# Kernel optimization log

Measured on AMD Instinct MI355X. Metric: run time of the kernel, lower is better.

The kernel has to match this reference:

```python
import jax, jax.numpy as jnp
import numpy as np

NUM_HEAD = 16
EMB_DIM = 1024
HEAD_DIM = EMB_DIM // NUM_HEAD

def setup_inputs() -> dict:
    key = jax.random.key(0)
    ks = jax.random.split(key, 9)
    B, S, D = 2, 2048, EMB_DIM
    s = 1.0 / np.sqrt(D)
    return {
        "x": jax.random.normal(ks[0], (B, S, D), dtype=jnp.float32),
        "Wq": jax.random.normal(ks[1], (D, D), dtype=jnp.float32) * s,
        "bq": jnp.zeros((D,), dtype=jnp.float32),
        "Wk": jax.random.normal(ks[2], (D, D), dtype=jnp.float32) * s,
        "bk": jnp.zeros((D,), dtype=jnp.float32),
        "Wv": jax.random.normal(ks[3], (D, D), dtype=jnp.float32) * s,
        "bv": jnp.zeros((D,), dtype=jnp.float32),
        "Wo": jax.random.normal(ks[4], (D, D), dtype=jnp.float32) * s,
        "bo": jnp.zeros((D,), dtype=jnp.float32),
    }

def reference(x, Wq, bq, Wk, bk, Wv, bv, Wo, bo):
    B, S, D = x.shape
    H, Hd = NUM_HEAD, HEAD_DIM
    # projections (torch Linear: x @ W.T + b; here W stored as [in, out])
    Q = (x @ Wq + bq).reshape(B, S, H, Hd)
    K = (x @ Wk + bk).reshape(B, S, H, Hd)
    V = (x @ Wv + bv).reshape(B, S, H, Hd)
    scale = jnp.sqrt(jnp.asarray(Hd, dtype=x.dtype))
    scores = jnp.einsum('bqhd,bkhd->bhqk', Q, K) / scale  # [B,H,S,S]
    attn = jax.nn.softmax(scores, axis=-1)
    out = jnp.einsum('bhql,blhd->bqhd', attn, V).reshape(B, S, D)
    return out @ Wo + bo
```

## Files before the change

kernel.cpp:

```cpp
#include <hip/hip_runtime.h>
#include <math.h>


using bf16   = __bf16;
using bf16x8 = __attribute__((ext_vector_type(8))) __bf16;
using bf16x4 = __attribute__((ext_vector_type(4))) __bf16;
using f32x4  = __attribute__((ext_vector_type(4))) float;

#define MFMA16(a, b, c) __builtin_amdgcn_mfma_f32_16x16x32_bf16((a), (b), (c), 0, 0, 0)
#define WAIT_VM0() asm volatile("s_waitcnt vmcnt(0)" ::: "memory")

__device__ __forceinline__ bf16x8 ld8(const bf16* p) { return *(const bf16x8*)p; }

__device__ __forceinline__ void ldg_lds16(bf16* lds_base, const bf16* g) {
    __builtin_amdgcn_global_load_lds(
        (const __attribute__((address_space(1))) void*)g,
        (__attribute__((address_space(3))) void*)lds_base, 16, 0, 0);
}

__device__ __forceinline__ float fast_exp2(float x) {
#if __has_builtin(__builtin_amdgcn_exp2f)
    return __builtin_amdgcn_exp2f(x);
#else
    return exp2f(x);
#endif
}

__device__ __forceinline__ float rowsum16(float v) {
    v += __shfl_xor(v, 1, 64);
    v += __shfl_xor(v, 2, 64);
    v += __shfl_xor(v, 4, 64);
    v += __shfl_xor(v, 8, 64);
    return v;
}

__global__ __launch_bounds__(256) void convert_x_kernel(const float* __restrict__ x,
                                                        bf16* __restrict__ xb) {
    int i = (blockIdx.x * 256 + threadIdx.x) * 4;
    float4 v = *(const float4*)&x[i];
    bf16x4 o = { (bf16)v.x, (bf16)v.y, (bf16)v.z, (bf16)v.w };
    *(bf16x4*)&xb[i] = o;
}

__global__ __launch_bounds__(256) void transpose_w_kernel(
    const float* __restrict__ Wq, const float* __restrict__ Wk,
    const float* __restrict__ Wv, const float* __restrict__ Wo,
    bf16* __restrict__ WtBase) {
    __shared__ float tile[32][33];
    const int z = blockIdx.z;
    const float* W = (z == 0) ? Wq : (z == 1) ? Wk : (z == 2) ? Wv : Wo;
    bf16* Wt = WtBase + (size_t)z * 1024 * 1024;
    const int tx = threadIdx.x, ty = threadIdx.y;
    const int x0 = blockIdx.x * 32, y0 = blockIdx.y * 32;
#pragma unroll
    for (int i = 0; i < 4; ++i)
        tile[ty + i * 8][tx] = W[(size_t)(y0 + ty + i * 8) * 1024 + x0 + tx];
    __syncthreads();
#pragma unroll
    for (int i = 0; i < 4; ++i)
        Wt[(size_t)(x0 + ty + i * 8) * 1024 + y0 + tx] = (bf16)tile[tx][ty + i * 8];
}

__device__ __forceinline__ void gemm_stage(const bf16* __restrict__ src, int r0,
                                           int k0, bf16* dst, int w, int lane) {
#pragma unroll
    for (int c = 0; c < 2; ++c) {
        int flat = (w * 2 + c) * 64 + lane;
        int row = flat >> 2, cc = flat & 3;
        int gk = (cc ^ ((row >> 1) & 3)) * 8;
        ldg_lds16(dst + (size_t)(w * 2 + c) * 512,
                  src + (size_t)(r0 + row) * 1024 + k0 + gk);
    }
}

__device__ __forceinline__ void gemm_core_128(const bf16* __restrict__ A,
                                              const bf16* __restrict__ Bt,
                                              int m0, int n0,
                                              bf16* As, bf16* Bs,
                                              f32x4 (&acc)[4][4]) {
    const int tid = threadIdx.x, lane = tid & 63, w = tid >> 6;
    const int lo = lane & 15, quad = lane >> 4;
    const int wm = w >> 1, wn = w & 1;

    gemm_stage(A,  m0, 0, As, w, lane);
    gemm_stage(Bt, n0, 0, Bs, w, lane);
    WAIT_VM0();
    __syncthreads();

    for (int it = 0; it < 32; ++it) {
        const int buf = it & 1;
        if (it + 1 < 32) {
            gemm_stage(A,  m0, (it + 1) * 32, As + (buf ^ 1) * 4096, w, lane);
            gemm_stage(Bt, n0, (it + 1) * 32, Bs + (buf ^ 1) * 4096, w, lane);
        }
        const bf16* Ab = As + buf * 4096;
        const bf16* Bb = Bs + buf * 4096;
        bf16x8 af[4], bq[4];
#pragma unroll
        for (int t = 0; t < 4; ++t) {
            int r = wm * 64 + t * 16 + lo;
            af[t] = ld8(&Ab[r * 32 + ((quad ^ ((r >> 1) & 3)) * 8)]);
        }
#pragma unroll
        for (int t = 0; t < 4; ++t) {
            int r = wn * 64 + t * 16 + lo;
            bq[t] = ld8(&Bb[r * 32 + ((quad ^ ((r >> 1) & 3)) * 8)]);
        }
#pragma unroll
        for (int mt = 0; mt < 4; ++mt)
#pragma unroll
            for (int nt = 0; nt < 4; ++nt)
                acc[mt][nt] = MFMA16(af[mt], bq[nt], acc[mt][nt]);
        WAIT_VM0();
        __syncthreads();
    }
}

__global__ __launch_bounds__(256, 3) void qkv_gemm_kernel(
    const bf16* __restrict__ Xb, const bf16* __restrict__ Wts,
    const float* __restrict__ bq, const float* __restrict__ bk,
    const float* __restrict__ bv,
    bf16* __restrict__ Qo, bf16* __restrict__ Ko, bf16* __restrict__ Vto) {
    __shared__ bf16 As[2 * 4096];
    __shared__ bf16 Bs[2 * 4096];
    const int z = blockIdx.z;
    const bf16*  Bt   = Wts + (size_t)z * 1024 * 1024;
    const float* bias = (z == 0) ? bq : (z == 1) ? bk : bv;
    const int m0 = blockIdx.y * 128, n0 = blockIdx.x * 128;

    f32x4 acc[4][4] = {};
    gemm_core_128(Xb, Bt, m0, n0, As, Bs, acc);

    const int lane = threadIdx.x & 63, w = threadIdx.x >> 6;
    const int lo = lane & 15, quad = lane >> 4;
    const int wm = w >> 1, wn = w & 1;
    const float QSCALE = 0.125f * 1.44269504088896f;
#pragma unroll
    for (int mt = 0; mt < 4; ++mt)
#pragma unroll
        for (int nt = 0; nt < 4; ++nt)
#pragma unroll
            for (int r = 0; r < 4; ++r) {
                int m = m0 + wm * 64 + mt * 16 + quad * 4 + r;
                int n = n0 + wn * 64 + nt * 16 + lo;
                float v = acc[mt][nt][r] + bias[n];
                int b = m >> 11, s = m & 2047, h = n >> 6, hd = n & 63;
                if (z == 0)
                    Qo[((size_t)((b * 16 + h) * 2048 + s) << 6) + hd] = (bf16)(v * QSCALE);
                else if (z == 1)
                    Ko[((size_t)((b * 16 + h) * 2048 + s) << 6) + hd] = (bf16)v;
                else
                    Vto[((size_t)((b * 16 + h) * 64 + hd) << 11) + s] = (bf16)v;
            }
}

__global__ __launch_bounds__(256, 3) void out_gemm_kernel(
    const bf16* __restrict__ Ab, const bf16* __restrict__ Bt,
    const float* __restrict__ bo, float* __restrict__ Co) {
    __shared__ bf16 As[2 * 4096];
    __shared__ bf16 Bs[2 * 4096];
    const int m0 = blockIdx.y * 128, n0 = blockIdx.x * 128;
    f32x4 acc[4][4] = {};
    gemm_core_128(Ab, Bt, m0, n0, As, Bs, acc);

    const int lane = threadIdx.x & 63, w = threadIdx.x >> 6;
    const int lo = lane & 15, quad = lane >> 4;
    const int wm = w >> 1, wn = w & 1;
#pragma unroll
    for (int mt = 0; mt < 4; ++mt)
#pragma unroll
        for (int nt = 0; nt < 4; ++nt)
#pragma unroll
            for (int r = 0; r < 4; ++r) {
                int m = m0 + wm * 64 + mt * 16 + quad * 4 + r;
                int n = n0 + wn * 64 + nt * 16 + lo;
                Co[(size_t)m * 1024 + n] = acc[mt][nt][r] + bo[n];
            }
}

#define PSTRIDE 72

__global__ __launch_bounds__(256, 2) void attn_kernel(
    const bf16* __restrict__ Q, const bf16* __restrict__ K,
    const bf16* __restrict__ Vt, bf16* __restrict__ AO) {
    __shared__ bf16 Ks[2][64 * 64];
    __shared__ bf16 Vs[2][64 * 64];
    __shared__ bf16 Pl[4][32 * PSTRIDE];
    const int tid = threadIdx.x, w = tid >> 6, lane = tid & 63;
    const int lo = lane & 15, quad = lane >> 4;
    const int blk = blockIdx.x;
    const int bh = (blk & 7) | ((blk >> 7) << 3);
    const int qb = (blk >> 3) & 15;
    const int q0 = qb * 128 + w * 32;

    const bf16* Qb = Q + ((size_t)bh * 2048 + q0) * 64;
    const bf16* Kb = K + (size_t)bh * 2048 * 64;
    const bf16* Vb = Vt + (size_t)bh * 64 * 2048;
    bf16* Pw = &Pl[w][0];

    bf16x8 qa[2][2];
#pragma unroll
    for (int mt = 0; mt < 2; ++mt)
#pragma unroll
        for (int ks = 0; ks < 2; ++ks)
            qa[mt][ks] = ld8(&Qb[(mt * 16 + lo) * 64 + ks * 32 + quad * 8]);

    f32x4 O[2][4] = {};
    f32x4 l_acc[2] = {};

    auto stage = [&](int s0, int buf) {
#pragma unroll
        for (int c = 0; c < 2; ++c) {
            int flat = (w * 2 + c) * 64 + lane;
            int row = flat >> 3, cc = flat & 7;
            int gK = (cc ^ ((row >> 2) & 7)) * 8;
            int gV = (cc ^ (row & 7)) * 8;
            ldg_lds16(&Ks[buf][(w * 2 + c) * 512], &Kb[(size_t)(s0 + row) * 64 + gK]);
            ldg_lds16(&Vs[buf][(w * 2 + c) * 512], &Vb[(size_t)row * 2048 + s0 + gV]);
        }
    };

    stage(0, 0);
    WAIT_VM0();
    __syncthreads();

    for (int it = 0; it < 32; ++it) {
        const int buf = it & 1;
        if (it + 1 < 32) stage((it + 1) * 64, buf ^ 1);
        const bf16* Kt = &Ks[buf][0];
        const bf16* Vl = &Vs[buf][0];

        f32x4 S[2][4] = {};
#pragma unroll
        for (int t = 0; t < 4; ++t) {
            int r = lo * 4 + t;
#pragma unroll
            for (int ks = 0; ks < 2; ++ks) {
                bf16x8 kf = ld8(&Kt[r * 64 + (((quad + 4 * ks) ^ ((r >> 2) & 7)) * 8)]);
                S[0][t] = MFMA16(qa[0][ks], kf, S[0][t]);
                S[1][t] = MFMA16(qa[1][ks], kf, S[1][t]);
            }
        }
#pragma unroll
        for (int mt = 0; mt < 2; ++mt)
#pragma unroll
            for (int r = 0; r < 4; ++r) {
                float p0 = fast_exp2(S[mt][0][r]);
                float p1 = fast_exp2(S[mt][1][r]);
                float p2 = fast_exp2(S[mt][2][r]);
                float p3 = fast_exp2(S[mt][3][r]);
                l_acc[mt][r] += (p0 + p1) + (p2 + p3);
                bf16x4 pk = { (bf16)p0, (bf16)p1, (bf16)p2, (bf16)p3 };
                *(bf16x4*)&Pw[(mt * 16 + quad * 4 + r) * PSTRIDE + lo * 4] = pk;
            }
#pragma unroll
        for (int mt = 0; mt < 2; ++mt) {
            bf16x8 pa0 = ld8(&Pw[(mt * 16 + lo) * PSTRIDE + quad * 8]);
            bf16x8 pa1 = ld8(&Pw[(mt * 16 + lo) * PSTRIDE + 32 + quad * 8]);
#pragma unroll
            for (int nt = 0; nt < 4; ++nt) {
                int r = nt * 16 + lo;
                bf16x8 v0 = ld8(&Vl[r * 64 + ((quad ^ (r & 7)) * 8)]);
                bf16x8 v1 = ld8(&Vl[r * 64 + (((quad + 4) ^ (r & 7)) * 8)]);
                O[mt][nt] = MFMA16(pa0, v0, O[mt][nt]);
                O[mt][nt] = MFMA16(pa1, v1, O[mt][nt]);
            }
        }
        WAIT_VM0();
        __syncthreads();
    }

    const int bb = bh >> 4, h = bh & 15;
#pragma unroll
    for (int mt = 0; mt < 2; ++mt) {
        const size_t outbase = ((size_t)(bb * 2048 + q0 + mt * 16)) * 1024 + h * 64;
#pragma unroll
        for (int r = 0; r < 4; ++r) {
            float rl = 1.0f / rowsum16(l_acc[mt][r]);
            size_t rowoff = outbase + (size_t)(quad * 4 + r) * 1024;
#pragma unroll
            for (int nt = 0; nt < 4; ++nt)
                AO[rowoff + nt * 16 + lo] = (bf16)(O[mt][nt][r] * rl);
        }
    }
}

extern "C" void kernel_launch(void* const* d_in, const int* in_sizes, int n_in,
                              void* d_out, int out_size, void* d_ws, size_t ws_size,
                              hipStream_t stream) {
    const float* x  = (const float*)d_in[0];
    const float* Wq = (const float*)d_in[1];
    const float* bq = (const float*)d_in[2];
    const float* Wk = (const float*)d_in[3];
    const float* bk = (const float*)d_in[4];
    const float* Wv = (const float*)d_in[5];
    const float* bv = (const float*)d_in[6];
    const float* Wo = (const float*)d_in[7];
    const float* bo = (const float*)d_in[8];
    float* out = (float*)d_out;

    bf16* wsb = (bf16*)d_ws;
    const size_t M1 = 1024u * 1024u;
    bf16* Xb  = wsb;
    bf16* AO  = wsb;
    bf16* Wt  = wsb + 4 * M1;
    bf16* Qw  = wsb + 8 * M1;
    bf16* Kw  = wsb + 12 * M1;
    bf16* Vtw = wsb + 16 * M1;

    convert_x_kernel<<<4096, 256, 0, stream>>>(x, Xb);
    transpose_w_kernel<<<dim3(32, 32, 4), dim3(32, 8), 0, stream>>>(Wq, Wk, Wv, Wo, Wt);
    qkv_gemm_kernel<<<dim3(8, 32, 3), 256, 0, stream>>>(Xb, Wt, bq, bk, bv, Qw, Kw, Vtw);
    attn_kernel<<<512, 256, 0, stream>>>(Qw, Kw, Vtw, AO);
    out_gemm_kernel<<<dim3(8, 32), 256, 0, stream>>>(AO, Wt + 3 * M1, bo, out);
}
```

Before: 203.7 us.

## Split attention into 128-thread blocks with shared V fragments and smaller P buffer

The attention kernel now runs 1024 blocks of two waves (64 query rows each) instead of 512 blocks of four waves. Each wave stages more of the K/V tile itself, and its probability scratch shrinks to one 16-row slab with a 68-element stride. That slab is reused for both 16-row halves. The V fragments are loaded from LDS once and reused for both halves, which cuts LDS reads. The cost is that every K/V tile is loaded from global memory by twice as many blocks, with fewer waves per block to hide latency.

```diff
diff --git a/kernel.cpp b/kernel.cpp
--- a/kernel.cpp
+++ b/kernel.cpp
@@ -178,20 +178,20 @@
             }
 }
 
-#define PSTRIDE 72
-
-__global__ __launch_bounds__(256, 2) void attn_kernel(
+#define PSTR 68
+
+__global__ __launch_bounds__(128, 2) void attn_kernel(
     const bf16* __restrict__ Q, const bf16* __restrict__ K,
     const bf16* __restrict__ Vt, bf16* __restrict__ AO) {
     __shared__ bf16 Ks[2][64 * 64];
     __shared__ bf16 Vs[2][64 * 64];
-    __shared__ bf16 Pl[4][32 * PSTRIDE];
+    __shared__ bf16 Pl[2][16 * PSTR];
     const int tid = threadIdx.x, w = tid >> 6, lane = tid & 63;
     const int lo = lane & 15, quad = lane >> 4;
     const int blk = blockIdx.x;
-    const int bh = (blk & 7) | ((blk >> 7) << 3);
-    const int qb = (blk >> 3) & 15;
-    const int q0 = qb * 128 + w * 32;
+    const int bh = (blk & 7) | ((blk >> 8) << 3);
+    const int qt = (blk >> 3) & 31;
+    const int q0 = qt * 64 + w * 32;
 
     const bf16* Qb = Q + ((size_t)bh * 2048 + q0) * 64;
     const bf16* Kb = K + (size_t)bh * 2048 * 64;
@@ -210,13 +210,14 @@
 
     auto stage = [&](int s0, int buf) {
 #pragma unroll
-        for (int c = 0; c < 2; ++c) {
-            int flat = (w * 2 + c) * 64 + lane;
+        for (int c = 0; c < 4; ++c) {
+            int slot = w * 4 + c;
+            int flat = slot * 64 + lane;
             int row = flat >> 3, cc = flat & 7;
             int gK = (cc ^ ((row >> 2) & 7)) * 8;
             int gV = (cc ^ (row & 7)) * 8;
-            ldg_lds16(&Ks[buf][(w * 2 + c) * 512], &Kb[(size_t)(s0 + row) * 64 + gK]);
-            ldg_lds16(&Vs[buf][(w * 2 + c) * 512], &Vb[(size_t)row * 2048 + s0 + gV]);
+            ldg_lds16(&Ks[buf][slot * 512], &Kb[(size_t)(s0 + row) * 64 + gK]);
+            ldg_lds16(&Vs[buf][slot * 512], &Vb[(size_t)row * 2048 + s0 + gV]);
         }
     };
 
@@ -242,28 +243,51 @@
             }
         }
 #pragma unroll
-        for (int mt = 0; mt < 2; ++mt)
-#pragma unroll
-            for (int r = 0; r < 4; ++r) {
-                float p0 = fast_exp2(S[mt][0][r]);
-                float p1 = fast_exp2(S[mt][1][r]);
-                float p2 = fast_exp2(S[mt][2][r]);
-                float p3 = fast_exp2(S[mt][3][r]);
-                l_acc[mt][r] += (p0 + p1) + (p2 + p3);
-                bf16x4 pk = { (bf16)p0, (bf16)p1, (bf16)p2, (bf16)p3 };
-                *(bf16x4*)&Pw[(mt * 16 + quad * 4 + r) * PSTRIDE + lo * 4] = pk;
-            }
-#pragma unroll
-        for (int mt = 0; mt < 2; ++mt) {
-            bf16x8 pa0 = ld8(&Pw[(mt * 16 + lo) * PSTRIDE + quad * 8]);
-            bf16x8 pa1 = ld8(&Pw[(mt * 16 + lo) * PSTRIDE + 32 + quad * 8]);
+        for (int r = 0; r < 4; ++r) {
+            float p0 = fast_exp2(S[0][0][r]);
+            float p1 = fast_exp2(S[0][1][r]);
+            float p2 = fast_exp2(S[0][2][r]);
+            float p3 = fast_exp2(S[0][3][r]);
+            l_acc[0][r] += (p0 + p1) + (p2 + p3);
+            bf16x4 pk = { (bf16)p0, (bf16)p1, (bf16)p2, (bf16)p3 };
+            *(bf16x4*)&Pw[(quad * 4 + r) * PSTR + lo * 4] = pk;
+        }
+        bf16x4 pk1[4];
+#pragma unroll
+        for (int r = 0; r < 4; ++r) {
+            float p0 = fast_exp2(S[1][0][r]);
+            float p1 = fast_exp2(S[1][1][r]);
+            float p2 = fast_exp2(S[1][2][r]);
+            float p3 = fast_exp2(S[1][3][r]);
+            l_acc[1][r] += (p0 + p1) + (p2 + p3);
+            pk1[r] = bf16x4{ (bf16)p0, (bf16)p1, (bf16)p2, (bf16)p3 };
+        }
+        bf16x8 vf0[4], vf1[4];
+#pragma unroll
+        for (int nt = 0; nt < 4; ++nt) {
+            int r = nt * 16 + lo;
+            vf0[nt] = ld8(&Vl[r * 64 + ((quad ^ (r & 7)) * 8)]);
+            vf1[nt] = ld8(&Vl[r * 64 + (((quad + 4) ^ (r & 7)) * 8)]);
+        }
+        {
+            bf16x8 pa0 = ld8(&Pw[lo * PSTR + quad * 8]);
+            bf16x8 pa1 = ld8(&Pw[lo * PSTR + 32 + quad * 8]);
 #pragma unroll
             for (int nt = 0; nt < 4; ++nt) {
-                int r = nt * 16 + lo;
-                bf16x8 v0 = ld8(&Vl[r * 64 + ((quad ^ (r & 7)) * 8)]);
-                bf16x8 v1 = ld8(&Vl[r * 64 + (((quad + 4) ^ (r & 7)) * 8)]);
-                O[mt][nt] = MFMA16(pa0, v0, O[mt][nt]);
-                O[mt][nt] = MFMA16(pa1, v1, O[mt][nt]);
+                O[0][nt] = MFMA16(pa0, vf0[nt], O[0][nt]);
+                O[0][nt] = MFMA16(pa1, vf1[nt], O[0][nt]);
+            }
+        }
+#pragma unroll
+        for (int r = 0; r < 4; ++r)
+            *(bf16x4*)&Pw[(quad * 4 + r) * PSTR + lo * 4] = pk1[r];
+        {
+            bf16x8 pa0 = ld8(&Pw[lo * PSTR + quad * 8]);
+            bf16x8 pa1 = ld8(&Pw[lo * PSTR + 32 + quad * 8]);
+#pragma unroll
+            for (int nt = 0; nt < 4; ++nt) {
+                O[1][nt] = MFMA16(pa0, vf0[nt], O[1][nt]);
+                O[1][nt] = MFMA16(pa1, vf1[nt], O[1][nt]);
             }
         }
         WAIT_VM0();
@@ -311,6 +335,6 @@
     convert_x_kernel<<<4096, 256, 0, stream>>>(x, Xb);
     transpose_w_kernel<<<dim3(32, 32, 4), dim3(32, 8), 0, stream>>>(Wq, Wk, Wv, Wo, Wt);
     qkv_gemm_kernel<<<dim3(8, 32, 3), 256, 0, stream>>>(Xb, Wt, bq, bk, bv, Qw, Kw, Vtw);
-    attn_kernel<<<512, 256, 0, stream>>>(Qw, Kw, Vtw, AO);
+    attn_kernel<<<1024, 128, 0, stream>>>(Qw, Kw, Vtw, AO);
     out_gemm_kernel<<<dim3(8, 32), 256, 0, stream>>>(AO, Wt + 3 * M1, bo, out);
 }
```

New measurement: 220.7 us. +8.3%, slower.

## Stage V-transpose epilogue through LDS and use 64-row tiles for output GEMM

Applied to the files above, without the earlier changes.

In the QKV projection, the V output (stored transposed) is now written by first staging each 64-row half of the tile transposed in shared memory, then emitting contiguous 4-element vector stores along the sequence dimension. This replaces scattered 2-byte strided stores. The output projection GEMM now uses a 64x128 tile with its own double-buffered loop, which doubles the grid to 512 blocks so the device's CUs are better covered. The trade-off is extra barriers and LDS traffic in the QKV epilogue, and less reuse per block in the output GEMM.

```diff
diff --git a/kernel.cpp b/kernel.cpp
--- a/kernel.cpp
+++ b/kernel.cpp
@@ -121,8 +121,9 @@
     const float* __restrict__ bq, const float* __restrict__ bk,
     const float* __restrict__ bv,
     bf16* __restrict__ Qo, bf16* __restrict__ Ko, bf16* __restrict__ Vto) {
-    __shared__ bf16 As[2 * 4096];
-    __shared__ bf16 Bs[2 * 4096];
+    __shared__ bf16 Smem[4 * 4096];
+    bf16* As = Smem;
+    bf16* Bs = Smem + 2 * 4096;
     const int z = blockIdx.z;
     const bf16*  Bt   = Wts + (size_t)z * 1024 * 1024;
     const float* bias = (z == 0) ? bq : (z == 1) ? bk : bv;
@@ -131,48 +132,129 @@
     f32x4 acc[4][4] = {};
     gemm_core_128(Xb, Bt, m0, n0, As, Bs, acc);
 
-    const int lane = threadIdx.x & 63, w = threadIdx.x >> 6;
+    const int tid = threadIdx.x;
+    const int lane = tid & 63, w = tid >> 6;
     const int lo = lane & 15, quad = lane >> 4;
     const int wm = w >> 1, wn = w & 1;
     const float QSCALE = 0.125f * 1.44269504088896f;
-#pragma unroll
-    for (int mt = 0; mt < 4; ++mt)
-#pragma unroll
-        for (int nt = 0; nt < 4; ++nt)
-#pragma unroll
-            for (int r = 0; r < 4; ++r) {
-                int m = m0 + wm * 64 + mt * 16 + quad * 4 + r;
-                int n = n0 + wn * 64 + nt * 16 + lo;
-                float v = acc[mt][nt][r] + bias[n];
-                int b = m >> 11, s = m & 2047, h = n >> 6, hd = n & 63;
-                if (z == 0)
-                    Qo[((size_t)((b * 16 + h) * 2048 + s) << 6) + hd] = (bf16)(v * QSCALE);
-                else if (z == 1)
-                    Ko[((size_t)((b * 16 + h) * 2048 + s) << 6) + hd] = (bf16)v;
-                else
-                    Vto[((size_t)((b * 16 + h) * 64 + hd) << 11) + s] = (bf16)v;
-            }
-}
-
-__global__ __launch_bounds__(256, 3) void out_gemm_kernel(
-    const bf16* __restrict__ Ab, const bf16* __restrict__ Bt,
+
+    if (z == 2) {
+        bf16* T = Smem;
+        const int b = m0 >> 11;
+        const int s_base = m0 & 2047;
+#pragma unroll
+        for (int half = 0; half < 2; ++half) {
+            __syncthreads();
+            if (wm == half) {
+#pragma unroll
+                for (int nt = 0; nt < 4; ++nt)
+#pragma unroll
+                    for (int mt = 0; mt < 4; ++mt)
+#pragma unroll
+                        for (int r = 0; r < 4; ++r) {
+                            int nn = wn * 64 + nt * 16 + lo;
+                            int mm = mt * 16 + quad * 4 + r;
+                            T[nn * 68 + mm] = (bf16)(acc[mt][nt][r] + bias[n0 + nn]);
+                        }
+            }
+            __syncthreads();
+#pragma unroll
+            for (int p = 0; p < 8; ++p) {
+                int pos = p * 1024 + tid * 4;
+                int row = pos >> 6, col = pos & 63;
+                int n = n0 + row, h = n >> 6, hd = n & 63;
+                bf16x4 v = *(const bf16x4*)&T[row * 68 + col];
+                *(bf16x4*)&Vto[((size_t)((b * 16 + h) * 64 + hd) << 11)
+                               + s_base + half * 64 + col] = v;
+            }
+        }
+    } else {
+#pragma unroll
+        for (int mt = 0; mt < 4; ++mt)
+#pragma unroll
+            for (int nt = 0; nt < 4; ++nt)
+#pragma unroll
+                for (int r = 0; r < 4; ++r) {
+                    int m = m0 + wm * 64 + mt * 16 + quad * 4 + r;
+                    int n = n0 + wn * 64 + nt * 16 + lo;
+                    float v = acc[mt][nt][r] + bias[n];
+                    int b = m >> 11, s = m & 2047, h = n >> 6, hd = n & 63;
+                    if (z == 0)
+                        Qo[((size_t)((b * 16 + h) * 2048 + s) << 6) + hd] = (bf16)(v * QSCALE);
+                    else
+                        Ko[((size_t)((b * 16 + h) * 2048 + s) << 6) + hd] = (bf16)v;
+                }
+    }
+}
+
+__global__ __launch_bounds__(256, 2) void out_gemm_kernel(
+    const bf16* __restrict__ A, const bf16* __restrict__ Bt,
     const float* __restrict__ bo, float* __restrict__ Co) {
-    __shared__ bf16 As[2 * 4096];
+    __shared__ bf16 As[2 * 2048];
     __shared__ bf16 Bs[2 * 4096];
-    const int m0 = blockIdx.y * 128, n0 = blockIdx.x * 128;
-    f32x4 acc[4][4] = {};
-    gemm_core_128(Ab, Bt, m0, n0, As, Bs, acc);
-
-    const int lane = threadIdx.x & 63, w = threadIdx.x >> 6;
+    const int tid = threadIdx.x, lane = tid & 63, w = tid >> 6;
     const int lo = lane & 15, quad = lane >> 4;
     const int wm = w >> 1, wn = w & 1;
-#pragma unroll
-    for (int mt = 0; mt < 4; ++mt)
+    const int m0 = blockIdx.y * 64, n0 = blockIdx.x * 128;
+
+    auto stageA = [&](int k0, bf16* dst) {
+        int flat = w * 64 + lane;
+        int row = flat >> 2, cc = flat & 3;
+        int gk = (cc ^ ((row >> 1) & 3)) * 8;
+        ldg_lds16(dst + (size_t)w * 512, A + (size_t)(m0 + row) * 1024 + k0 + gk);
+    };
+    auto stageB = [&](int k0, bf16* dst) {
+#pragma unroll
+        for (int c = 0; c < 2; ++c) {
+            int flat = (w * 2 + c) * 64 + lane;
+            int row = flat >> 2, cc = flat & 3;
+            int gk = (cc ^ ((row >> 1) & 3)) * 8;
+            ldg_lds16(dst + (size_t)(w * 2 + c) * 512,
+                      Bt + (size_t)(n0 + row) * 1024 + k0 + gk);
+        }
+    };
+
+    f32x4 acc[2][4] = {};
+    stageA(0, As);
+    stageB(0, Bs);
+    WAIT_VM0();
+    __syncthreads();
+
+    for (int it = 0; it < 32; ++it) {
+        const int buf = it & 1;
+        if (it + 1 < 32) {
+            stageA((it + 1) * 32, As + (buf ^ 1) * 2048);
+            stageB((it + 1) * 32, Bs + (buf ^ 1) * 4096);
+        }
+        const bf16* Ab = As + buf * 2048;
+        const bf16* Bb = Bs + buf * 4096;
+        bf16x8 af[2], bq[4];
+#pragma unroll
+        for (int t = 0; t < 2; ++t) {
+            int r = wm * 32 + t * 16 + lo;
+            af[t] = ld8(&Ab[r * 32 + ((quad ^ ((r >> 1) & 3)) * 8)]);
+        }
+#pragma unroll
+        for (int t = 0; t < 4; ++t) {
+            int r = wn * 64 + t * 16 + lo;
+            bq[t] = ld8(&Bb[r * 32 + ((quad ^ ((r >> 1) & 3)) * 8)]);
+        }
+#pragma unroll
+        for (int mt = 0; mt < 2; ++mt)
+#pragma unroll
+            for (int nt = 0; nt < 4; ++nt)
+                acc[mt][nt] = MFMA16(af[mt], bq[nt], acc[mt][nt]);
+        WAIT_VM0();
+        __syncthreads();
+    }
+
+#pragma unroll
+    for (int mt = 0; mt < 2; ++mt)
 #pragma unroll
         for (int nt = 0; nt < 4; ++nt)
 #pragma unroll
             for (int r = 0; r < 4; ++r) {
-                int m = m0 + wm * 64 + mt * 16 + quad * 4 + r;
+                int m = m0 + wm * 32 + mt * 16 + quad * 4 + r;
                 int n = n0 + wn * 64 + nt * 16 + lo;
                 Co[(size_t)m * 1024 + n] = acc[mt][nt][r] + bo[n];
             }
@@ -312,5 +394,5 @@
     transpose_w_kernel<<<dim3(32, 32, 4), dim3(32, 8), 0, stream>>>(Wq, Wk, Wv, Wo, Wt);
     qkv_gemm_kernel<<<dim3(8, 32, 3), 256, 0, stream>>>(Xb, Wt, bq, bk, bv, Qw, Kw, Vtw);
     attn_kernel<<<512, 256, 0, stream>>>(Qw, Kw, Vtw, AO);
-    out_gemm_kernel<<<dim3(8, 32), 256, 0, stream>>>(AO, Wt + 3 * M1, bo, out);
-}
+    out_gemm_kernel<<<dim3(8, 64), 256, 0, stream>>>(AO, Wt + 3 * M1, bo, out);
+}
```

Result: faster. 191.1 us (-6.2%).
